# Optimization experiments

Measured on AMD Instinct MI355X. Metric: run time of the kernel, lower is better.

Reference implementation:

```python
import jax, jax.numpy as jnp
import numpy as np

N_NODES = 10000
N_EDGES = 80000
TILE, EMB, HID, OUT = 32, 128, 256, 512


def setup_inputs() -> dict:
    key = jax.random.key(0)
    ks = jax.random.split(key, 20)
    s = 0.05
    inp = {
        'x': jax.random.normal(ks[0], (N_NODES, TILE), dtype=jnp.float32),
        'edge_index': jax.random.randint(ks[1], (2, N_EDGES), 0, N_NODES, dtype=jnp.int64),
        # input_proj (spectral_norm Linear -> treated as a plain normalized weight)
        'W_in': jax.random.normal(ks[2], (TILE, EMB), dtype=jnp.float32) * s,
        'b_in': jnp.zeros((EMB,), dtype=jnp.float32),
        # GATConv 1: 128 -> 256, heads=8
        'W1': jax.random.normal(ks[3], (EMB, 8 * HID), dtype=jnp.float32) * s,
        'as1': jax.random.normal(ks[4], (8, HID), dtype=jnp.float32) * s,
        'ad1': jax.random.normal(ks[5], (8, HID), dtype=jnp.float32) * s,
        'b1': jnp.zeros((8 * HID,), dtype=jnp.float32),
        # GATConv 2: 2048 -> 256, heads=8
        'W2': jax.random.normal(ks[6], (8 * HID, 8 * HID), dtype=jnp.float32) * s,
        'as2': jax.random.normal(ks[7], (8, HID), dtype=jnp.float32) * s,
        'ad2': jax.random.normal(ks[8], (8, HID), dtype=jnp.float32) * s,
        'b2': jnp.zeros((8 * HID,), dtype=jnp.float32),
        # GATConv 3: 2048 -> 512, heads=1
        'W3': jax.random.normal(ks[9], (8 * HID, OUT), dtype=jnp.float32) * s,
        'as3': jax.random.normal(ks[10], (1, OUT), dtype=jnp.float32) * s,
        'ad3': jax.random.normal(ks[11], (1, OUT), dtype=jnp.float32) * s,
        'b3': jnp.zeros((OUT,), dtype=jnp.float32),
    }
    return inp


def _gat(x, src, dst, W, a_src, a_dst, bias, heads, ch):
    # x: [N, F_in]; src/dst: [E_tot] (self loops included)
    n = x.shape[0]
    h = (x @ W).reshape(n, heads, ch)                      # [N, H, C]
    alpha_src = jnp.sum(h * a_src, axis=-1)                # [N, H]
    alpha_dst = jnp.sum(h * a_dst, axis=-1)                # [N, H]
    e = jax.nn.leaky_relu(alpha_src[src] + alpha_dst[dst], 0.2)  # [E, H]
    # segment softmax over destination nodes
    m = jax.ops.segment_max(e, dst, num_segments=n)
    ex = jnp.exp(e - m[dst])
    denom = jax.ops.segment_sum(ex, dst, num_segments=n)
    alpha = ex / (denom[dst] + 1e-16)                      # [E, H]
    out = jax.ops.segment_sum(h[src] * alpha[:, :, None], dst, num_segments=n)
    return out.reshape(n, heads * ch) + bias


def reference(x, edge_index, W_in, b_in, W1, as1, ad1, b1, W2, as2, ad2, b2, W3, as3, ad3, b3):
    n = x.shape[0]
    lr = lambda t: jax.nn.leaky_relu(t, 0.2)
    # PyG GATConv adds self-loops by default
    loops = jnp.arange(n, dtype=edge_index.dtype)
    src = jnp.concatenate([edge_index[0], loops])
    dst = jnp.concatenate([edge_index[1], loops])
    h = lr(x @ W_in + b_in)
    h = lr(_gat(h, src, dst, W1, as1, ad1, b1, 8, HID))
    h = lr(_gat(h, src, dst, W2, as2, ad2, b2, 8, HID))
    h = lr(_gat(h, src, dst, W3, as3, ad3, b3, 1, OUT))
    return h
```

## Files before the change

### kernel.cpp

```cpp
#include <hip/hip_runtime.h>

typedef unsigned short u16;
typedef unsigned int u32;
typedef _Float16 f16;
typedef f16 f16x8 __attribute__((ext_vector_type(8)));
typedef float f32x4 __attribute__((ext_vector_type(4)));

__device__ __forceinline__ float h2f(f16 h){ return (float)h; }
__device__ __forceinline__ f16 f2h(float f){ return (f16)f; }

__device__ __forceinline__ f16x8 ldfrag(const f16* p){
  union { uint4 u; f16x8 h; } x;
  x.u = *(const uint4*)p;
  return x.h;
}
__device__ __forceinline__ void gload_lds16(const f16* g, f16* l){
  __builtin_amdgcn_global_load_lds(
      (const __attribute__((address_space(1))) u32*)g,
      (__attribute__((address_space(3))) u32*)l, 16, 0, 0);
}


__global__ void detect_kernel(const int* __restrict__ ei, int* __restrict__ flag){
  if (threadIdx.x == 0 && blockIdx.x == 0){
    int orv = 0;
    for (int i = 0; i < 200; i++) orv |= ei[2*i + 1];
    *flag = (orv == 0) ? 1 : 0;
  }
}

__global__ void init_kernel(int* __restrict__ cnt, int* __restrict__ fillpos, int n){
  int i = blockIdx.x * blockDim.x + threadIdx.x;
  if (i < n){ cnt[i] = 1; fillpos[i] = 1; }
}

__global__ void count_edges(const int* __restrict__ ei, int E, const int* __restrict__ flag,
                            int* __restrict__ cnt){
  int e = blockIdx.x * blockDim.x + threadIdx.x;
  if (e >= E) return;
  int dst = (*flag) ? ei[2*E + 2*e] : ei[E + e];
  atomicAdd(&cnt[dst], 1);
}

#define SCAN_T 1024
__global__ void scan_kernel(const int* __restrict__ cnt, int* __restrict__ row_ptr, int n){
  __shared__ int sm[SCAN_T];
  int t = threadIdx.x;
  int chunk = (n + SCAN_T - 1) / SCAN_T;
  int lo = t * chunk, hi = lo + chunk; if (hi > n) hi = n; if (lo > n) lo = n;
  int s = 0;
  for (int i = lo; i < hi; i++) s += cnt[i];
  sm[t] = s; __syncthreads();
  for (int off = 1; off < SCAN_T; off <<= 1){
    int v = (t >= off) ? sm[t - off] : 0;
    __syncthreads();
    sm[t] += v;
    __syncthreads();
  }
  int base = sm[t] - s;
  for (int i = lo; i < hi; i++){ row_ptr[i] = base; base += cnt[i]; }
  if (t == 0) row_ptr[n] = sm[SCAN_T - 1];
}

__global__ void selfloop_kernel(const int* __restrict__ row_ptr, int* __restrict__ col, int n){
  int i = blockIdx.x * blockDim.x + threadIdx.x;
  if (i < n) col[row_ptr[i]] = i;
}

__global__ void fill_edges(const int* __restrict__ ei, int E, const int* __restrict__ flag,
                           const int* __restrict__ row_ptr, int* __restrict__ fillpos,
                           int* __restrict__ col){
  int e = blockIdx.x * blockDim.x + threadIdx.x;
  if (e >= E) return;
  int f = *flag;
  int src = f ? ei[2*e]       : ei[e];
  int dst = f ? ei[2*E + 2*e] : ei[E + e];
  int off = atomicAdd(&fillpos[dst], 1);
  col[row_ptr[dst] + off] = src;
}


__global__ void convert_f16(const float* __restrict__ X, f16* __restrict__ Xo, long n){
  long i = blockIdx.x * (long)blockDim.x + threadIdx.x;
  if (i >= n) return;
  Xo[i] = f2h(X[i]);
}

__global__ void convert_wT(const float* __restrict__ W, f16* __restrict__ T, int K, int N){
  __shared__ float sm[32][33];
  int kb = blockIdx.x * 32, nb = blockIdx.y * 32;
  int tx = threadIdx.x, ty = threadIdx.y;
  for (int i = 0; i < 32; i += 8)
    sm[ty + i][tx] = W[(size_t)(kb + ty + i) * N + nb + tx];
  __syncthreads();
  for (int i = 0; i < 32; i += 8)
    T[(size_t)(nb + ty + i) * K + kb + tx] = f2h(sm[tx][ty + i]);
}


template<int EPI, int FJ>
__global__ __launch_bounds__(256) void gemm_kernel(
    const f16* __restrict__ A, const f16* __restrict__ B,
    float* __restrict__ C, f16* __restrict__ Ch,
    const float* __restrict__ bias,
    int M, int N, int K, int nbm, int nbn)
{
  constexpr int BN = FJ * 32;
  __shared__ f16 sA[2][128 * 32];
  __shared__ f16 sB[2][BN * 32];

  int nwg = nbm * nbn;
  int bid = blockIdx.x;
  int q = nwg >> 3, r = nwg & 7;
  int xcd = bid & 7, idx = bid >> 3;
  int wg = (xcd < r ? xcd * (q + 1) : r * (q + 1) + (xcd - r) * q) + idx;
  int bm = wg / nbn, bn = wg % nbn;

  int tid = threadIdx.x;
  int lane = tid & 63;
  int w = tid >> 6;
  int wr = (w >> 1) * 64, wc = (w & 1) * (FJ * 16);
  int lm = lane & 15;

  int sk = (((tid & 3) ^ ((tid >> 3) & 3))) * 8;
  int phys8 = (((lane >> 4) ^ ((lm >> 1) & 3))) * 8;

  long ar0 = (long)bm * 128 + (tid >> 2);
  long ar1 = ar0 + 64;
  if (ar0 >= M) ar0 = M - 1;
  if (ar1 >= M) ar1 = M - 1;
  long br0 = (long)bn * BN + (tid >> 2);
  long br1 = br0 + 64;

  const f16* pA0 = A + ar0 * K + sk;
  const f16* pA1 = A + ar1 * K + sk;
  const f16* pB0 = B + br0 * K + sk;
  const f16* pB1 = (FJ == 4) ? (B + br1 * K + sk) : pB0;
  const int d1 = 2048;

  auto STAGE = [&](int buf, int k0){
    gload_lds16(pA0 + k0, &sA[buf][tid * 8]);
    gload_lds16(pA1 + k0, &sA[buf][d1 + tid * 8]);
    gload_lds16(pB0 + k0, &sB[buf][tid * 8]);
    if constexpr (FJ == 4)
      gload_lds16(pB1 + k0, &sB[buf][d1 + tid * 8]);
  };

  f32x4 acc[4][FJ] = {};

  int nt = K >> 5;
  STAGE(0, 0);
  __syncthreads();
  int cur = 0;
  for (int t = 0; t < nt; t++){
    if (t + 1 < nt) STAGE(cur ^ 1, (t + 1) * 32);
    f16x8 af[4], bfr[FJ];
    #pragma unroll
    for (int f = 0; f < 4; f++)
      af[f] = ldfrag(&sA[cur][(wr + f * 16 + lm) * 32 + phys8]);
    #pragma unroll
    for (int f = 0; f < FJ; f++)
      bfr[f] = ldfrag(&sB[cur][(wc + f * 16 + lm) * 32 + phys8]);
    #pragma unroll
    for (int fi = 0; fi < 4; fi++)
      #pragma unroll
      for (int fj = 0; fj < FJ; fj++)
        acc[fi][fj] = __builtin_amdgcn_mfma_f32_16x16x32_f16(af[fi], bfr[fj], acc[fi][fj], 0, 0, 0);
    __syncthreads();
    cur ^= 1;
  }

  #pragma unroll
  for (int fi = 0; fi < 4; fi++){
    int mb = bm * 128 + wr + fi * 16 + ((lane >> 4) << 2);
    #pragma unroll
    for (int fj = 0; fj < FJ; fj++){
      int n = bn * BN + wc + fj * 16 + lm;
      #pragma unroll
      for (int j = 0; j < 4; j++){
        int m = mb + j;
        if (m < M){
          float v = acc[fi][fj][j];
          size_t o = (size_t)m * N + n;
          if (EPI == 0){
            C[o] = v;
          } else if (EPI == 2){
            Ch[o] = f2h(v);
          } else {
            v += bias[n];
            v = v > 0.0f ? v : 0.2f * v;
            Ch[o] = f2h(v);
          }
        }
      }
    }
  }
}


template<int HEADS, int CH>
__global__ __launch_bounds__(256) void alpha_kernel(
    const f16* __restrict__ H, const float* __restrict__ a_s, const float* __restrict__ a_d,
    float* __restrict__ asrc, float* __restrict__ adst, int Nn)
{
  int gw = blockIdx.x * 4 + (threadIdx.x >> 6);
  int lane = threadIdx.x & 63;
  int node = gw / HEADS, hd = gw % HEADS;
  if (node >= Nn) return;
  size_t base = (size_t)node * HEADS * CH + hd * CH;
  const float* asp = a_s + hd * CH;
  const float* adp = a_d + hd * CH;
  float s1 = 0.0f, s2 = 0.0f;
  #pragma unroll
  for (int i = 0; i < CH / 256; i++){
    int off = i * 256 + lane * 4;
    union { uint2 u; f16 h[4]; } x;
    x.u = *(const uint2*)(H + base + off);
    float4 s4 = *(const float4*)(asp + off);
    float4 d4 = *(const float4*)(adp + off);
    s1 += h2f(x.h[0]) * s4.x + h2f(x.h[1]) * s4.y + h2f(x.h[2]) * s4.z + h2f(x.h[3]) * s4.w;
    s2 += h2f(x.h[0]) * d4.x + h2f(x.h[1]) * d4.y + h2f(x.h[2]) * d4.z + h2f(x.h[3]) * d4.w;
  }
  for (int off = 32; off; off >>= 1){
    s1 += __shfl_xor(s1, off);
    s2 += __shfl_xor(s2, off);
  }
  if (lane == 0){ asrc[gw] = s1; adst[gw] = s2; }
}


template<int HEADS, int CH, bool FINAL>
__global__ __launch_bounds__(256) void smax_agg_kernel(
    const f16* __restrict__ H, const int* __restrict__ row_ptr,
    const int* __restrict__ col,
    const float* __restrict__ asrc, const float* __restrict__ adst,
    const float* __restrict__ bias, f16* __restrict__ Oh, float* __restrict__ Ofp)
{
  constexpr int F = HEADS * CH;
  constexpr int CPT = F / 256;
  __shared__ float s_m[HEADS], s_inv[HEADS];
  int dst = blockIdx.x;
  int t = threadIdx.x;
  int s = row_ptr[dst], e = row_ptr[dst + 1];

  if (t < 64){
    const int hd = (HEADS == 8) ? (t & 7) : 0;
    const int el = (HEADS == 8) ? (t >> 3) : t;
    const int EPP = 64 / HEADS;
    float ad = adst[dst * HEADS + hd];
    float m = -1e30f;
    for (int p = s + el; p < e; p += EPP){
      float v = asrc[col[p] * HEADS + hd] + ad;
      v = v > 0.0f ? v : 0.2f * v;
      m = fmaxf(m, v);
    }
    for (int off = HEADS; off < 64; off <<= 1) m = fmaxf(m, __shfl_xor(m, off));
    float sum = 0.0f;
    for (int p = s + el; p < e; p += EPP){
      float v = asrc[col[p] * HEADS + hd] + ad;
      v = v > 0.0f ? v : 0.2f * v;
      sum += __expf(v - m);
    }
    for (int off = HEADS; off < 64; off <<= 1) sum += __shfl_xor(sum, off);
    if (el == 0){ s_m[hd] = m; s_inv[hd] = 1.0f / (sum + 1e-16f); }
  }
  __syncthreads();

  int c0 = t * CPT;
  int hd = c0 / CH;
  float m = s_m[hd], inv = s_inv[hd];
  float ad = adst[dst * HEADS + hd];
  float acc[CPT] = {};
  int p = s;

  auto wgt = [&](int src) -> float {
    float v = asrc[src * HEADS + hd] + ad;
    v = v > 0.0f ? v : 0.2f * v;
    return __expf(v - m) * inv;
  };

  for (; p + 4 <= e; p += 4){
    int i0 = col[p], i1 = col[p+1], i2 = col[p+2], i3 = col[p+3];
    if (CPT == 8){
      union { uint4 u; f16 h[8]; } x0, x1, x2, x3;
      x0.u = *(const uint4*)(H + (size_t)i0 * F + c0);
      x1.u = *(const uint4*)(H + (size_t)i1 * F + c0);
      x2.u = *(const uint4*)(H + (size_t)i2 * F + c0);
      x3.u = *(const uint4*)(H + (size_t)i3 * F + c0);
      float w0 = wgt(i0), w1 = wgt(i1), w2 = wgt(i2), w3 = wgt(i3);
      #pragma unroll
      for (int i = 0; i < 8; i++)
        acc[i] += w0 * h2f(x0.h[i]) + w1 * h2f(x1.h[i])
                + w2 * h2f(x2.h[i]) + w3 * h2f(x3.h[i]);
    } else {
      union { u32 u; f16 h[2]; } x0, x1, x2, x3;
      x0.u = *(const u32*)(H + (size_t)i0 * F + c0);
      x1.u = *(const u32*)(H + (size_t)i1 * F + c0);
      x2.u = *(const u32*)(H + (size_t)i2 * F + c0);
      x3.u = *(const u32*)(H + (size_t)i3 * F + c0);
      float w0 = wgt(i0), w1 = wgt(i1), w2 = wgt(i2), w3 = wgt(i3);
      acc[0] += w0 * h2f(x0.h[0]) + w1 * h2f(x1.h[0]) + w2 * h2f(x2.h[0]) + w3 * h2f(x3.h[0]);
      acc[1] += w0 * h2f(x0.h[1]) + w1 * h2f(x1.h[1]) + w2 * h2f(x2.h[1]) + w3 * h2f(x3.h[1]);
    }
  }
  for (; p < e; p++){
    int src = col[p];
    float w0 = wgt(src);
    if (CPT == 8){
      union { uint4 u; f16 h[8]; } x;
      x.u = *(const uint4*)(H + (size_t)src * F + c0);
      #pragma unroll
      for (int i = 0; i < 8; i++) acc[i] += w0 * h2f(x.h[i]);
    } else {
      union { u32 u; f16 h[2]; } x;
      x.u = *(const u32*)(H + (size_t)src * F + c0);
      acc[0] += w0 * h2f(x.h[0]); acc[1] += w0 * h2f(x.h[1]);
    }
  }

  #pragma unroll
  for (int i = 0; i < CPT; i++){
    float v = acc[i] + bias[c0 + i];
    v = v > 0.0f ? v : 0.2f * v;
    size_t o = (size_t)dst * F + c0 + i;
    if (FINAL) Ofp[o] = v;
    else       Oh[o]  = f2h(v);
  }
}


extern "C" void kernel_launch(void* const* d_in, const int* in_sizes, int n_in,
                              void* d_out, int out_size, void* d_ws, size_t ws_size,
                              hipStream_t stream)
{
  const float* x    = (const float*)d_in[0];
  const int*   ei   = (const int*)d_in[1];
  const float* W_in = (const float*)d_in[2];
  const float* b_in = (const float*)d_in[3];
  const float* W1   = (const float*)d_in[4];
  const float* as1  = (const float*)d_in[5];
  const float* ad1  = (const float*)d_in[6];
  const float* b1   = (const float*)d_in[7];
  const float* W2   = (const float*)d_in[8];
  const float* as2  = (const float*)d_in[9];
  const float* ad2  = (const float*)d_in[10];
  const float* b2   = (const float*)d_in[11];
  const float* W3   = (const float*)d_in[12];
  const float* as3  = (const float*)d_in[13];
  const float* ad3  = (const float*)d_in[14];
  const float* b3   = (const float*)d_in[15];

  const int N  = in_sizes[0] / 32;
  const int E  = in_sizes[1] / 2;
  const int ET = E + N;

  char* w = (char*)d_ws;
  size_t off = 0;
  auto carve = [&](size_t bytes) -> char* {
    off = (off + 255) & ~(size_t)255;
    char* p = w + off;
    off += bytes;
    return p;
  };

  int* flag    = (int*)carve(4);
  int* cnt     = (int*)carve((size_t)N * 4);
  int* fillpos = (int*)carve((size_t)N * 4);
  int* row_ptr = (int*)carve((size_t)(N + 1) * 4);
  int* col     = (int*)carve((size_t)ET * 4);
  f16* xh      = (f16*)carve((size_t)N * 32 * 2);
  f16* h0      = (f16*)carve((size_t)N * 128 * 2);
  f16* WT      = (f16*)carve((size_t)2048 * 2048 * 2);
  f16* Hb      = (f16*)carve((size_t)N * 2048 * 2);
  f16* H3      = (f16*)carve((size_t)N * 512 * 2);
  f16* XB      = (f16*)carve((size_t)N * 2048 * 2);
  float* asrc  = (float*)carve((size_t)N * 8 * 4);
  float* adst  = (float*)carve((size_t)N * 8 * 4);

  if (off > ws_size) return;

  const int MT = (N + 127) / 128;
  float* out = (float*)d_out;

  detect_kernel<<<1, 1, 0, stream>>>(ei, flag);
  init_kernel<<<(N + 255) / 256, 256, 0, stream>>>(cnt, fillpos, N);
  count_edges<<<(E + 255) / 256, 256, 0, stream>>>(ei, E, flag, cnt);
  scan_kernel<<<1, SCAN_T, 0, stream>>>(cnt, row_ptr, N);
  selfloop_kernel<<<(N + 255) / 256, 256, 0, stream>>>(row_ptr, col, N);
  fill_edges<<<(E + 255) / 256, 256, 0, stream>>>(ei, E, flag, row_ptr, fillpos, col);

  convert_f16<<<((long)N * 32 + 255) / 256, 256, 0, stream>>>(x, xh, (long)N * 32);
  convert_wT<<<dim3(1, 4), dim3(32, 8), 0, stream>>>(W_in, WT, 32, 128);
  gemm_kernel<1, 4><<<MT * 1, 256, 0, stream>>>(xh, WT, nullptr, h0, b_in,
      N, 128, 32, MT, 1);

  convert_wT<<<dim3(4, 64), dim3(32, 8), 0, stream>>>(W1, WT, 128, 2048);
  gemm_kernel<2, 4><<<MT * 16, 256, 0, stream>>>(h0, WT, nullptr, Hb, nullptr,
      N, 2048, 128, MT, 16);
  alpha_kernel<8, 256><<<(N * 8 + 3) / 4, 256, 0, stream>>>(Hb, as1, ad1, asrc, adst, N);
  smax_agg_kernel<8, 256, false><<<N, 256, 0, stream>>>(Hb, row_ptr, col,
      asrc, adst, b1, XB, nullptr);

  convert_wT<<<dim3(64, 64), dim3(32, 8), 0, stream>>>(W2, WT, 2048, 2048);
  gemm_kernel<2, 4><<<MT * 16, 256, 0, stream>>>(XB, WT, nullptr, Hb, nullptr,
      N, 2048, 2048, MT, 16);
  alpha_kernel<8, 256><<<(N * 8 + 3) / 4, 256, 0, stream>>>(Hb, as2, ad2, asrc, adst, N);
  smax_agg_kernel<8, 256, false><<<N, 256, 0, stream>>>(Hb, row_ptr, col,
      asrc, adst, b2, XB, nullptr);

  convert_wT<<<dim3(64, 16), dim3(32, 8), 0, stream>>>(W3, WT, 2048, 512);
  gemm_kernel<2, 2><<<MT * 8, 256, 0, stream>>>(XB, WT, nullptr, H3, nullptr,
      N, 512, 2048, MT, 8);
  alpha_kernel<1, 512><<<(N + 3) / 4, 256, 0, stream>>>(H3, as3, ad3, asrc, adst, N);
  smax_agg_kernel<1, 512, true><<<N, 256, 0, stream>>>(H3, row_ptr, col,
      asrc, adst, b3, nullptr, out);
}
```

Before: 390.1 us.

## Deepen GEMM K-tile to 64 with new LDS swizzle and padded M buffers

```diff
diff --git a/kernel.cpp b/kernel.cpp
--- a/kernel.cpp
+++ b/kernel.cpp
@@ -98,16 +98,22 @@
 }
 
 
-template<int EPI, int FJ>
+template<int EPI, int FJ, int BK>
 __global__ __launch_bounds__(256) void gemm_kernel(
     const f16* __restrict__ A, const f16* __restrict__ B,
     float* __restrict__ C, f16* __restrict__ Ch,
     const float* __restrict__ bias,
     int M, int N, int K, int nbm, int nbn)
 {
-  constexpr int BN = FJ * 32;
-  __shared__ f16 sA[2][128 * 32];
-  __shared__ f16 sB[2][BN * 32];
+  constexpr int BN  = FJ * 32;
+  constexpr int TPR = BK / 8;
+  constexpr int RPG = 256 / TPR;
+  constexpr int NGA = 128 / RPG;
+  constexpr int NGB = BN / RPG;
+  constexpr int KS  = BK / 32;
+
+  __shared__ f16 sA[2][128 * BK];
+  __shared__ f16 sB[2][BN * BK];
 
   int nwg = nbm * nbn;
   int bid = blockIdx.x;
@@ -122,50 +128,67 @@
   int wr = (w >> 1) * 64, wc = (w & 1) * (FJ * 16);
   int lm = lane & 15;
 
-  int sk = (((tid & 3) ^ ((tid >> 3) & 3))) * 8;
-  int phys8 = (((lane >> 4) ^ ((lm >> 1) & 3))) * 8;
-
-  long ar0 = (long)bm * 128 + (tid >> 2);
-  long ar1 = ar0 + 64;
-  if (ar0 >= M) ar0 = M - 1;
-  if (ar1 >= M) ar1 = M - 1;
-  long br0 = (long)bn * BN + (tid >> 2);
-  long br1 = br0 + 64;
-
-  const f16* pA0 = A + ar0 * K + sk;
-  const f16* pA1 = A + ar1 * K + sk;
-  const f16* pB0 = B + br0 * K + sk;
-  const f16* pB1 = (FJ == 4) ? (B + br1 * K + sk) : pB0;
-  const int d1 = 2048;
+  int slot = tid % TPR, rg = tid / TPR;
+  int sk;
+  if constexpr (BK == 64) sk = ((slot ^ (rg & 7))) * 8;
+  else                    sk = ((slot ^ ((rg >> 1) & 3))) * 8;
+
+  const f16* pA[NGA];
+  const f16* pB[NGB];
+  #pragma unroll
+  for (int i = 0; i < NGA; i++)
+    pA[i] = A + ((long)bm * 128 + rg + RPG * i) * K + sk;
+  #pragma unroll
+  for (int i = 0; i < NGB; i++)
+    pB[i] = B + ((long)bn * BN + rg + RPG * i) * K + sk;
 
   auto STAGE = [&](int buf, int k0){
-    gload_lds16(pA0 + k0, &sA[buf][tid * 8]);
-    gload_lds16(pA1 + k0, &sA[buf][d1 + tid * 8]);
-    gload_lds16(pB0 + k0, &sB[buf][tid * 8]);
-    if constexpr (FJ == 4)
-      gload_lds16(pB1 + k0, &sB[buf][d1 + tid * 8]);
+    #pragma unroll
+    for (int i = 0; i < NGA; i++)
+      gload_lds16(pA[i] + k0, &sA[buf][i * 2048 + tid * 8]);
+    #pragma unroll
+    for (int i = 0; i < NGB; i++)
+      gload_lds16(pB[i] + k0, &sB[buf][i * 2048 + tid * 8]);
   };
 
   f32x4 acc[4][FJ] = {};
 
-  int nt = K >> 5;
+  int nt = K / BK;
   STAGE(0, 0);
   __syncthreads();
   int cur = 0;
   for (int t = 0; t < nt; t++){
-    if (t + 1 < nt) STAGE(cur ^ 1, (t + 1) * 32);
-    f16x8 af[4], bfr[FJ];
+    if (t + 1 < nt) STAGE(cur ^ 1, (t + 1) * BK);
+    f16x8 af[4][KS], bfr[FJ][KS];
     #pragma unroll
-    for (int f = 0; f < 4; f++)
-      af[f] = ldfrag(&sA[cur][(wr + f * 16 + lm) * 32 + phys8]);
+    for (int ks = 0; ks < KS; ks++){
+      #pragma unroll
+      for (int f = 0; f < 4; f++){
+        int row = wr + f * 16 + lm;
+        int phys;
+        if constexpr (BK == 64) phys = (ks * 4 + (lane >> 4)) ^ (lm & 7);
+        else                    phys = (lane >> 4) ^ ((lm >> 1) & 3);
+        af[f][ks] = ldfrag(&sA[cur][row * BK + phys * 8]);
+      }
+      #pragma unroll
+      for (int f = 0; f < FJ; f++){
+        int row = wc + f * 16 + lm;
+        int phys;
+        if constexpr (BK == 64) phys = (ks * 4 + (lane >> 4)) ^ (lm & 7);
+        else                    phys = (lane >> 4) ^ ((lm >> 1) & 3);
+        bfr[f][ks] = ldfrag(&sB[cur][row * BK + phys * 8]);
+      }
+    }
+    __builtin_amdgcn_s_setprio(1);
     #pragma unroll
-    for (int f = 0; f < FJ; f++)
-      bfr[f] = ldfrag(&sB[cur][(wc + f * 16 + lm) * 32 + phys8]);
-    #pragma unroll
-    for (int fi = 0; fi < 4; fi++)
-      #pragma unroll
-      for (int fj = 0; fj < FJ; fj++)
-        acc[fi][fj] = __builtin_amdgcn_mfma_f32_16x16x32_f16(af[fi], bfr[fj], acc[fi][fj], 0, 0, 0);
+    for (int ks = 0; ks < KS; ks++)
+      #pragma unroll
+      for (int fi = 0; fi < 4; fi++)
+        #pragma unroll
+        for (int fj = 0; fj < FJ; fj++)
+          acc[fi][fj] = __builtin_amdgcn_mfma_f32_16x16x32_f16(
+              af[fi][ks], bfr[fj][ks], acc[fi][fj], 0, 0, 0);
+    __builtin_amdgcn_s_setprio(0);
     __syncthreads();
     cur ^= 1;
   }
@@ -179,18 +202,16 @@
       #pragma unroll
       for (int j = 0; j < 4; j++){
         int m = mb + j;
-        if (m < M){
-          float v = acc[fi][fj][j];
-          size_t o = (size_t)m * N + n;
-          if (EPI == 0){
-            C[o] = v;
-          } else if (EPI == 2){
-            Ch[o] = f2h(v);
-          } else {
-            v += bias[n];
-            v = v > 0.0f ? v : 0.2f * v;
-            Ch[o] = f2h(v);
-          }
+        float v = acc[fi][fj][j];
+        size_t o = (size_t)m * N + n;
+        if (EPI == 0){
+          C[o] = v;
+        } else if (EPI == 2){
+          Ch[o] = f2h(v);
+        } else {
+          v += bias[n];
+          v = v > 0.0f ? v : 0.2f * v;
+          Ch[o] = f2h(v);
         }
       }
     }
@@ -353,6 +374,8 @@
   const int N  = in_sizes[0] / 32;
   const int E  = in_sizes[1] / 2;
   const int ET = E + N;
+  const int MT = (N + 127) / 128;
+  const int MP = MT * 128;
 
   char* w = (char*)d_ws;
   size_t off = 0;
@@ -368,18 +391,17 @@
   int* fillpos = (int*)carve((size_t)N * 4);
   int* row_ptr = (int*)carve((size_t)(N + 1) * 4);
   int* col     = (int*)carve((size_t)ET * 4);
-  f16* xh      = (f16*)carve((size_t)N * 32 * 2);
-  f16* h0      = (f16*)carve((size_t)N * 128 * 2);
+  f16* xh      = (f16*)carve((size_t)MP * 32 * 2);
+  f16* h0      = (f16*)carve((size_t)MP * 128 * 2);
   f16* WT      = (f16*)carve((size_t)2048 * 2048 * 2);
-  f16* Hb      = (f16*)carve((size_t)N * 2048 * 2);
-  f16* H3      = (f16*)carve((size_t)N * 512 * 2);
-  f16* XB      = (f16*)carve((size_t)N * 2048 * 2);
+  f16* Hb      = (f16*)carve((size_t)MP * 2048 * 2);
+  f16* H3      = (f16*)carve((size_t)MP * 512 * 2);
+  f16* XB      = (f16*)carve((size_t)MP * 2048 * 2);
   float* asrc  = (float*)carve((size_t)N * 8 * 4);
   float* adst  = (float*)carve((size_t)N * 8 * 4);
 
   if (off > ws_size) return;
 
-  const int MT = (N + 127) / 128;
   float* out = (float*)d_out;
 
   detect_kernel<<<1, 1, 0, stream>>>(ei, flag);
@@ -391,26 +413,26 @@
 
   convert_f16<<<((long)N * 32 + 255) / 256, 256, 0, stream>>>(x, xh, (long)N * 32);
   convert_wT<<<dim3(1, 4), dim3(32, 8), 0, stream>>>(W_in, WT, 32, 128);
-  gemm_kernel<1, 4><<<MT * 1, 256, 0, stream>>>(xh, WT, nullptr, h0, b_in,
-      N, 128, 32, MT, 1);
+  gemm_kernel<1, 4, 32><<<MT * 1, 256, 0, stream>>>(xh, WT, nullptr, h0, b_in,
+      MP, 128, 32, MT, 1);
 
   convert_wT<<<dim3(4, 64), dim3(32, 8), 0, stream>>>(W1, WT, 128, 2048);
-  gemm_kernel<2, 4><<<MT * 16, 256, 0, stream>>>(h0, WT, nullptr, Hb, nullptr,
-      N, 2048, 128, MT, 16);
+  gemm_kernel<2, 4, 64><<<MT * 16, 256, 0, stream>>>(h0, WT, nullptr, Hb, nullptr,
+      MP, 2048, 128, MT, 16);
   alpha_kernel<8, 256><<<(N * 8 + 3) / 4, 256, 0, stream>>>(Hb, as1, ad1, asrc, adst, N);
   smax_agg_kernel<8, 256, false><<<N, 256, 0, stream>>>(Hb, row_ptr, col,
       asrc, adst, b1, XB, nullptr);
 
   convert_wT<<<dim3(64, 64), dim3(32, 8), 0, stream>>>(W2, WT, 2048, 2048);
-  gemm_kernel<2, 4><<<MT * 16, 256, 0, stream>>>(XB, WT, nullptr, Hb, nullptr,
-      N, 2048, 2048, MT, 16);
+  gemm_kernel<2, 4, 64><<<MT * 16, 256, 0, stream>>>(XB, WT, nullptr, Hb, nullptr,
+      MP, 2048, 2048, MT, 16);
   alpha_kernel<8, 256><<<(N * 8 + 3) / 4, 256, 0, stream>>>(Hb, as2, ad2, asrc, adst, N);
   smax_agg_kernel<8, 256, false><<<N, 256, 0, stream>>>(Hb, row_ptr, col,
       asrc, adst, b2, XB, nullptr);
 
   convert_wT<<<dim3(64, 16), dim3(32, 8), 0, stream>>>(W3, WT, 2048, 512);
-  gemm_kernel<2, 2><<<MT * 8, 256, 0, stream>>>(XB, WT, nullptr, H3, nullptr,
-      N, 512, 2048, MT, 8);
+  gemm_kernel<2, 2, 64><<<MT * 8, 256, 0, stream>>>(XB, WT, nullptr, H3, nullptr,
+      MP, 512, 2048, MT, 8);
   alpha_kernel<1, 512><<<(N + 3) / 4, 256, 0, stream>>>(H3, as3, ad3, asrc, adst, N);
   smax_agg_kernel<1, 512, true><<<N, 256, 0, stream>>>(H3, row_ptr, col,
       asrc, adst, b3, nullptr, out);
```

After: 372.4 us. 1.05x faster.
